# Performance work log

Measured on AMD Instinct MI355X. Metric: run time of the kernel, lower is better.

Reference implementation:

```python
import jax, jax.numpy as jnp
import numpy as np

B, S, H, D, M = 4, 512, 768, 24, 96
OUT_HID = 2 * max(128, H // 2)  # 768

def setup_inputs() -> dict:
    key = jax.random.key(0)
    ks = jax.random.split(key, 10)
    g = lambda k, shp, s=0.02: (jax.random.normal(k, shp, jnp.float32) * s)
    return {
        'H_j': jax.random.normal(ks[0], (B, S, H), jnp.float32),
        'H_i': jax.random.normal(ks[1], (B, S, H), jnp.float32),
        'attn_mask': jnp.ones((B, S), jnp.float32),
        'p_j_w': g(ks[2], (D, H)),
        'p_i_w': g(ks[3], (D, H)),
        's_w1': g(ks[4], (M, 4 * D)),
        's_b1': jnp.zeros((M,), jnp.float32),
        's_w2': g(ks[5], (1, M)),
        's_b2': jnp.zeros((1,), jnp.float32),
        'v_w1': g(ks[6], (OUT_HID, 3 * H)),
        'v_b1': jnp.zeros((OUT_HID,), jnp.float32),
        'v_w2': g(ks[7], (H, OUT_HID)),
        'v_b2': jnp.zeros((H,), jnp.float32),
        'alpha': jnp.asarray(0.05, jnp.float32),
    }

def reference(H_j, H_i, attn_mask, p_j_w, p_i_w, s_w1, s_b1, s_w2, s_b2,
              v_w1, v_b1, v_w2, v_b2, alpha):
    # Projections: [B,S,D]
    Zj = H_j @ p_j_w.T
    Zi = H_i @ p_i_w.T
    # score_mlp layer1 on concat([Zj_pair, Zi_pair, hadam, |diff|]) ==
    # sum of the 4 block-matmuls (block-split of W1 over the concat axis).
    Wa, Wb, Wc, Wd = jnp.split(s_w1, 4, axis=1)        # each [M, D]
    Zj_p = Zj[:, :, None, :]                            # [B,S,1,D]
    Zi_p = Zi[:, None, :, :]                            # [B,1,S,D]
    hid = (jnp.einsum('bsd,md->bsm', Zj, Wa)[:, :, None, :]
           + jnp.einsum('btd,md->btm', Zi, Wb)[:, None, :, :]
           + jnp.einsum('bstd,md->bstm', Zj_p * Zi_p, Wc)
           + jnp.einsum('bstd,md->bstm', jnp.abs(Zj_p - Zi_p), Wd)
           + s_b1)                                      # [B,S,S,M]
    logits = jnp.einsum('bstm,om->bst', jax.nn.relu(hid), s_w2)[..., :] + s_b2[0]  # [B,S,S]
    neg = jnp.finfo(logits.dtype).min
    logits = logits + (1.0 - attn_mask)[:, None, :] * neg  # mask over keys
    probs = jax.nn.softmax(logits, axis=-1)
    ctx = jnp.einsum('bst,bth->bsh', probs, H_i)           # [B,S,H]
    msg_in = jnp.concatenate([ctx, H_j, ctx * H_j], axis=-1)  # concat_hadam: [B,S,3H]
    msg = jax.nn.relu(msg_in @ v_w1.T + v_b1) @ v_w2.T + v_b2
    return alpha * msg  # dropout is identity in eval mode
```

## Files before the change

kernel.cpp:

```cpp
#include <hip/hip_runtime.h>
#include <hip/hip_bf16.h>
#include <math.h>

#define BB 4
#define SS 512
#define HH 768
#define DD 24
#define MM 96
#define OH 768
#define K3H 2304

typedef unsigned short u16;
typedef unsigned int u32;
typedef short bf16x8 __attribute__((ext_vector_type(8)));
typedef float f32x4 __attribute__((ext_vector_type(4)));
typedef u16 u16x4 __attribute__((ext_vector_type(4)));

#define OFF_A     0
#define F32_END   (OFF_A + BB*SS*MM)
#define MB_MSGIN  0
#define MB_H1     (MB_MSGIN + BB*SS*K3H)
#define MB_W1     (MB_H1    + BB*SS*OH)
#define MB_W2     (MB_W1    + OH*K3H)
#define MB_PROBS  (MB_W2    + OH*HH)
#define MB_HIT    (MB_PROBS + BB*SS*SS)
#define MB_ZJP    (MB_HIT   + BB*HH*SS)
#define MB_ZIP    (MB_ZJP   + BB*SS*32)
#define MB_WM     (MB_ZIP   + BB*SS*32)

__device__ inline u16 f2bf(float x) {
    union { float f; u32 u; } v; v.f = x;
    u32 r = v.u + 0x7fffu + ((v.u >> 16) & 1u);
    return (u16)(r >> 16);
}
__device__ inline u32 pk2bf(float lo, float hi) {
    return ((__float_as_uint(lo) + 0x8000u) >> 16) |
           ((__float_as_uint(hi) + 0x8000u) & 0xffff0000u);
}
__device__ inline void unpack8(bf16x8 v, float* f) {
    const u32* d = (const u32*)&v;
    #pragma unroll
    for (int i = 0; i < 4; ++i) {
        f[2*i]   = __uint_as_float(d[i] << 16);
        f[2*i+1] = __uint_as_float(d[i] & 0xffff0000u);
    }
}
__device__ inline void gl_lds16(const u16* g, u16* l) {
    __builtin_amdgcn_global_load_lds(
        (const __attribute__((address_space(1))) void*)g,
        (__attribute__((address_space(3))) void*)l, 16, 0, 0);
}

__global__ __launch_bounds__(256) void k_zproj(
    const float* __restrict__ Hj, const float* __restrict__ Hi,
    const float* __restrict__ pjw, const float* __restrict__ piw,
    const float* __restrict__ sw1, const float* __restrict__ sb1,
    u16* __restrict__ Zjp, u16* __restrict__ Zip, float* __restrict__ A)
{
    int bs = blockIdx.x;
    __shared__ float hj[HH], hi[HH], zj[DD], zi[DD];
    int tid = threadIdx.x;
    for (int i = tid; i < HH; i += 256) {
        hj[i] = Hj[(size_t)bs*HH + i];
        hi[i] = Hi[(size_t)bs*HH + i];
    }
    __syncthreads();
    int wid = tid >> 6, lane = tid & 63;
    for (int o = wid; o < 2*DD; o += 4) {
        int isJ = (o < DD); int d = isJ ? o : o - DD;
        const float* w = (isJ ? pjw : piw) + (size_t)d * HH;
        const float* x = isJ ? hj : hi;
        float acc = 0.f;
        #pragma unroll
        for (int k = 0; k < HH/64; ++k) { int h = lane + 64*k; acc = fmaf(x[h], w[h], acc); }
        #pragma unroll
        for (int off = 32; off > 0; off >>= 1) acc += __shfl_down(acc, off);
        if (lane == 0) { if (isJ) zj[d] = acc; else zi[d] = acc; }
    }
    __syncthreads();
    if (tid < 32)      Zjp[(size_t)bs*32 + tid] = (tid < DD) ? f2bf(zj[tid]) : (u16)0;
    else if (tid < 64) { int c = tid - 32; Zip[(size_t)bs*32 + c] = (c < DD) ? f2bf(zi[c]) : (u16)0; }
    if (tid < MM) {
        float acc = sb1[tid];
        #pragma unroll
        for (int d = 0; d < DD; ++d) acc = fmaf(zj[d], sw1[tid*96 + d], acc);
        A[(size_t)bs*MM + tid] = acc;
    }
}

__global__ __launch_bounds__(256) void k_wprep(
    const float* __restrict__ sw1, const float* __restrict__ vw1,
    const float* __restrict__ vw2,
    u16* __restrict__ Wm, u16* __restrict__ w1b, u16* __restrict__ w2b)
{
    int bx = blockIdx.x;
    if (bx == 0) {
        for (int i = threadIdx.x; i < MM*96; i += 256) {
            int m = i / 96, k = i % 96;
            float v = 0.f;
            if (k < 24)                 v = sw1[m*96 + 48 + k];
            else if (k >= 32 && k < 56) v = sw1[m*96 + 72 + (k - 32)];
            else if (k >= 64 && k < 88) v = sw1[m*96 + 24 + (k - 64)];
            Wm[i] = f2bf(v);
        }
        return;
    }
    int idx = bx - 1;
    const float* src; u16* dst;
    if (idx < 864) { src = vw1; dst = w1b; }
    else           { idx -= 864; src = vw2; dst = w2b; }
    int i = (idx*256 + threadIdx.x) * 8;
    float4 a = *(const float4*)&src[i];
    float4 c = *(const float4*)&src[i+4];
    u16x4 lo = { f2bf(a.x), f2bf(a.y), f2bf(a.z), f2bf(a.w) };
    u16x4 hi = { f2bf(c.x), f2bf(c.y), f2bf(c.z), f2bf(c.w) };
    *(u16x4*)&dst[i]   = lo;
    *(u16x4*)&dst[i+4] = hi;
}

__global__ __launch_bounds__(256) void k_pair_mfma(
    const u16* __restrict__ Zjp, const u16* __restrict__ Zip,
    const float* __restrict__ A, const u16* __restrict__ Wm,
    const float* __restrict__ sw2, const float* __restrict__ mask,
    u16* __restrict__ probsb)
{
    int blk = blockIdx.x; int b = blk >> 8; int s0 = (blk & 255) * 2;
    int tid = threadIdx.x, wave = tid >> 6, lane = tid & 63;
    int q = lane >> 4, l16 = lane & 15;
    int si = wave & 1, half = wave >> 1;
    int s = s0 + si, bs = b*SS + s;
    __shared__ __align__(16) u16 ZiS[SS*32];
    __shared__ float logits[2][SS];

    {
        const u16* zb = Zip + (size_t)b*SS*32;
        #pragma unroll
        for (int p = 0; p < 8; ++p) {
            int idx = p*256 + tid;
            int t = idx >> 2, c = idx & 3;
            int g = c ^ ((t + (t >> 2)) & 3);
            gl_lds16(zb + t*32 + g*8, ZiS + idx*8);
        }
    }

    bf16x8 zjf = *(const bf16x8*)&Zjp[(size_t)bs*32 + q*8];
    float zj[8]; unpack8(zjf, zj);
    bf16x8 afc[6], afd[6];
    #pragma unroll
    for (int mt = 0; mt < 6; ++mt) {
        const u16* wrow = &Wm[(mt*16 + l16)*96];
        bf16x8 wcf = *(const bf16x8*)&wrow[q*8];
        afd[mt]    = *(const bf16x8*)&wrow[32 + q*8];
        bf16x8 wbf = *(const bf16x8*)&wrow[64 + q*8];
        float fc[8], fb[8];
        unpack8(wcf, fc); unpack8(wbf, fb);
        u32 aval = (u32)f2bf(A[(size_t)bs*MM + mt*16 + l16]);
        union { u32 d[4]; bf16x8 v; } pk;
        #pragma unroll
        for (int i = 0; i < 4; ++i)
            pk.d[i] = pk2bf(fmaf(fc[2*i], zj[2*i], fb[2*i]),
                            fmaf(fc[2*i+1], zj[2*i+1], fb[2*i+1]));
        pk.d[0] = (q == 3) ? aval : pk.d[0];
        afc[mt] = pk.v;
    }
    float w2v[6][4];
    #pragma unroll
    for (int mt = 0; mt < 6; ++mt)
        #pragma unroll
        for (int r = 0; r < 4; ++r) w2v[mt][r] = sw2[mt*16 + q*4 + r];

    __syncthreads();

    for (int k = 0; k < 16; ++k) {
        int t0 = (half*16 + k) * 16;
        int trow = t0 + l16;
        int sw = q ^ ((trow + (trow >> 2)) & 3);
        bf16x8 zif = *(const bf16x8*)&ZiS[trow*32 + sw*8];
        float zi[8]; unpack8(zif, zi);
        union { u32 d[4]; bf16x8 v; } b1, b2;
        #pragma unroll
        for (int i = 0; i < 4; ++i)
            b1.d[i] = pk2bf(fabsf(zj[2*i] - zi[2*i]), fabsf(zj[2*i+1] - zi[2*i+1]));
        b2.v = zif;
        b2.d[0] = (q == 3) ? 0x3F80u : b2.d[0];
        f32x4 acc[6];
        #pragma unroll
        for (int mt = 0; mt < 6; ++mt) {
            f32x4 a = {};
            a = __builtin_amdgcn_mfma_f32_16x16x32_bf16(afc[mt], b2.v, a, 0,0,0);
            a = __builtin_amdgcn_mfma_f32_16x16x32_bf16(afd[mt], b1.v, a, 0,0,0);
            acc[mt] = a;
        }
        float p = 0.f;
        #pragma unroll
        for (int mt = 0; mt < 6; ++mt)
            #pragma unroll
            for (int r = 0; r < 4; ++r)
                p = fmaf(fmaxf(acc[mt][r], 0.f), w2v[mt][r], p);
        p += __shfl_xor(p, 16);
        p += __shfl_xor(p, 32);
        if (lane < 16) logits[si][t0 + lane] = p;
    }
    __syncthreads();

    if (wave < 2) {
        const float NEGF = -3.4028234663852886e38f;
        int bss = b*SS + s0 + wave;
        float l[8], e[8];
        float mx = -INFINITY;
        #pragma unroll
        for (int i = 0; i < 8; ++i) {
            int idx = lane + i*64;
            l[i] = logits[wave][idx] + (1.f - mask[b*SS + idx]) * NEGF;
            mx = fmaxf(mx, l[i]);
        }
        #pragma unroll
        for (int off = 32; off > 0; off >>= 1) mx = fmaxf(mx, __shfl_xor(mx, off));
        float sum = 0.f;
        #pragma unroll
        for (int i = 0; i < 8; ++i) { e[i] = __expf(l[i] - mx); sum += e[i]; }
        #pragma unroll
        for (int off = 32; off > 0; off >>= 1) sum += __shfl_xor(sum, off);
        float inv = 1.f / sum;
        #pragma unroll
        for (int i = 0; i < 8; ++i)
            probsb[(size_t)bss*SS + lane + i*64] = f2bf(e[i] * inv);
    }
}

__global__ __launch_bounds__(256) void k_hit(
    const float* __restrict__ Hi, u16* __restrict__ HiTb)
{
    int b = blockIdx.z; int t0 = blockIdx.x * 32; int h0 = blockIdx.y * 32;
    __shared__ float tile[32][33];
    int tx = threadIdx.x & 31, ty = threadIdx.x >> 5;
    for (int i = ty; i < 32; i += 8)
        tile[i][tx] = Hi[((size_t)(b*SS) + t0 + i)*HH + h0 + tx];
    __syncthreads();
    for (int i = ty; i < 32; i += 8)
        HiTb[((size_t)b*HH + h0 + i)*SS + t0 + tx] = f2bf(tile[tx][i]);
}

__global__ __launch_bounds__(256) void k_ctx_mfma(
    const u16* __restrict__ probsb, const u16* __restrict__ HiTb,
    const float* __restrict__ Hj, u16* __restrict__ msginb)
{
    int b = blockIdx.z;
    int h0 = blockIdx.x * 64;
    int s0 = blockIdx.y * 64;
    int tid = threadIdx.x;
    __shared__ __align__(16) u16 As[64*32];
    __shared__ __align__(16) u16 Bs[64*32];
    int row = tid >> 2, cs = tid & 3;
    int gchunk = cs ^ ((row >> 1) & 3);
    int wave = tid >> 6, lane = tid & 63;
    int wr = (wave >> 1) * 32, wc = (wave & 1) * 32;
    int q = lane >> 4, l16 = lane & 15;
    int sA = (l16 >> 1) & 3;
    f32x4 acc00 = {}, acc01 = {}, acc10 = {}, acc11 = {};
    const u16* ag = probsb + ((size_t)(b*SS) + s0 + row)*SS + gchunk*8;
    const u16* bg = HiTb + ((size_t)b*HH + h0 + row)*SS + gchunk*8;
    u16* lA = As + tid*8;
    u16* lB = Bs + tid*8;
    for (int k0 = 0; k0 < SS; k0 += 32) {
        gl_lds16(ag + k0, lA);
        gl_lds16(bg + k0, lB);
        __syncthreads();
        bf16x8 a0 = *(const bf16x8*)&As[(wr      + l16)*32 + (q^sA)*8];
        bf16x8 a1 = *(const bf16x8*)&As[(wr + 16 + l16)*32 + (q^sA)*8];
        bf16x8 b0 = *(const bf16x8*)&Bs[(wc      + l16)*32 + (q^sA)*8];
        bf16x8 b1 = *(const bf16x8*)&Bs[(wc + 16 + l16)*32 + (q^sA)*8];
        acc00 = __builtin_amdgcn_mfma_f32_16x16x32_bf16(a0, b0, acc00, 0,0,0);
        acc01 = __builtin_amdgcn_mfma_f32_16x16x32_bf16(a0, b1, acc01, 0,0,0);
        acc10 = __builtin_amdgcn_mfma_f32_16x16x32_bf16(a1, b0, acc10, 0,0,0);
        acc11 = __builtin_amdgcn_mfma_f32_16x16x32_bf16(a1, b1, acc11, 0,0,0);
        __syncthreads();
    }
    #pragma unroll
    for (int rt = 0; rt < 2; ++rt) {
        #pragma unroll
        for (int ct = 0; ct < 2; ++ct) {
            const f32x4* ac = rt ? (ct ? &acc11 : &acc10) : (ct ? &acc01 : &acc00);
            int h = h0 + wc + ct*16 + l16;
            #pragma unroll
            for (int r = 0; r < 4; ++r) {
                int s = s0 + wr + rt*16 + q*4 + r;
                float v = (*ac)[r];
                float hj = Hj[((size_t)(b*SS) + s)*HH + h];
                u16* mb = msginb + (size_t)(b*SS + s)*K3H + h;
                mb[0]    = f2bf(v);
                mb[HH]   = f2bf(hj);
                mb[2*HH] = f2bf(v * hj);
            }
        }
    }
}

__global__ __launch_bounds__(256) void k_mfma_gemm1(
    const u16* __restrict__ Abf, const u16* __restrict__ Bbf,
    const float* __restrict__ bias, u16* __restrict__ Cbf)
{
    int o0 = blockIdx.x * 64;
    int n0 = blockIdx.y * 64;
    int tid = threadIdx.x;
    __shared__ __align__(16) u16 As[64*32];
    __shared__ __align__(16) u16 Bs[64*32];
    int row = tid >> 2, cs = tid & 3;
    int gchunk = cs ^ ((row >> 1) & 3);
    int wave = tid >> 6, lane = tid & 63;
    int wr = (wave >> 1) * 32, wc = (wave & 1) * 32;
    int q = lane >> 4, l16 = lane & 15;
    int sA = (l16 >> 1) & 3;
    f32x4 acc00 = {}, acc01 = {}, acc10 = {}, acc11 = {};
    const u16* ag = Abf + (size_t)(n0 + row)*K3H + gchunk*8;
    const u16* bg = Bbf + (size_t)(o0 + row)*K3H + gchunk*8;
    u16* lA = As + tid*8;
    u16* lB = Bs + tid*8;
    for (int k0 = 0; k0 < K3H; k0 += 32) {
        gl_lds16(ag + k0, lA);
        gl_lds16(bg + k0, lB);
        __syncthreads();
        bf16x8 a0 = *(const bf16x8*)&As[(wr      + l16)*32 + (q^sA)*8];
        bf16x8 a1 = *(const bf16x8*)&As[(wr + 16 + l16)*32 + (q^sA)*8];
        bf16x8 b0 = *(const bf16x8*)&Bs[(wc      + l16)*32 + (q^sA)*8];
        bf16x8 b1 = *(const bf16x8*)&Bs[(wc + 16 + l16)*32 + (q^sA)*8];
        acc00 = __builtin_amdgcn_mfma_f32_16x16x32_bf16(a0, b0, acc00, 0,0,0);
        acc01 = __builtin_amdgcn_mfma_f32_16x16x32_bf16(a0, b1, acc01, 0,0,0);
        acc10 = __builtin_amdgcn_mfma_f32_16x16x32_bf16(a1, b0, acc10, 0,0,0);
        acc11 = __builtin_amdgcn_mfma_f32_16x16x32_bf16(a1, b1, acc11, 0,0,0);
        __syncthreads();
    }
    #pragma unroll
    for (int rt = 0; rt < 2; ++rt) {
        #pragma unroll
        for (int ct = 0; ct < 2; ++ct) {
            const f32x4* ac = rt ? (ct ? &acc11 : &acc10) : (ct ? &acc01 : &acc00);
            int o = o0 + wc + ct*16 + l16;
            float bv = bias[o];
            #pragma unroll
            for (int r = 0; r < 4; ++r) {
                int m = n0 + wr + rt*16 + q*4 + r;
                Cbf[(size_t)m*OH + o] = f2bf(fmaxf((*ac)[r] + bv, 0.f));
            }
        }
    }
}

__global__ __launch_bounds__(256) void k_mfma_gemm2(
    const u16* __restrict__ Abf, const u16* __restrict__ Bbf,
    const float* __restrict__ bias, const float* __restrict__ alpha,
    float* __restrict__ out)
{
    int o0 = blockIdx.x * 64;
    int n0 = blockIdx.y * 64;
    int tid = threadIdx.x;
    __shared__ __align__(16) u16 As[64*32];
    __shared__ __align__(16) u16 Bs[64*32];
    int row = tid >> 2, cs = tid & 3;
    int gchunk = cs ^ ((row >> 1) & 3);
    int wave = tid >> 6, lane = tid & 63;
    int wr = (wave >> 1) * 32, wc = (wave & 1) * 32;
    int q = lane >> 4, l16 = lane & 15;
    int sA = (l16 >> 1) & 3;
    f32x4 acc00 = {}, acc01 = {}, acc10 = {}, acc11 = {};
    const u16* ag = Abf + (size_t)(n0 + row)*OH + gchunk*8;
    const u16* bg = Bbf + (size_t)(o0 + row)*OH + gchunk*8;
    u16* lA = As + tid*8;
    u16* lB = Bs + tid*8;
    for (int k0 = 0; k0 < OH; k0 += 32) {
        gl_lds16(ag + k0, lA);
        gl_lds16(bg + k0, lB);
        __syncthreads();
        bf16x8 a0 = *(const bf16x8*)&As[(wr      + l16)*32 + (q^sA)*8];
        bf16x8 a1 = *(const bf16x8*)&As[(wr + 16 + l16)*32 + (q^sA)*8];
        bf16x8 b0 = *(const bf16x8*)&Bs[(wc      + l16)*32 + (q^sA)*8];
        bf16x8 b1 = *(const bf16x8*)&Bs[(wc + 16 + l16)*32 + (q^sA)*8];
        acc00 = __builtin_amdgcn_mfma_f32_16x16x32_bf16(a0, b0, acc00, 0,0,0);
        acc01 = __builtin_amdgcn_mfma_f32_16x16x32_bf16(a0, b1, acc01, 0,0,0);
        acc10 = __builtin_amdgcn_mfma_f32_16x16x32_bf16(a1, b0, acc10, 0,0,0);
        acc11 = __builtin_amdgcn_mfma_f32_16x16x32_bf16(a1, b1, acc11, 0,0,0);
        __syncthreads();
    }
    float al = alpha[0];
    #pragma unroll
    for (int rt = 0; rt < 2; ++rt) {
        #pragma unroll
        for (int ct = 0; ct < 2; ++ct) {
            const f32x4* ac = rt ? (ct ? &acc11 : &acc10) : (ct ? &acc01 : &acc00);
            int o = o0 + wc + ct*16 + l16;
            float bv = bias[o];
            #pragma unroll
            for (int r = 0; r < 4; ++r) {
                int m = n0 + wr + rt*16 + q*4 + r;
                out[(size_t)m*HH + o] = al * ((*ac)[r] + bv);
            }
        }
    }
}

extern "C" void kernel_launch(void* const* d_in, const int* in_sizes, int n_in,
                              void* d_out, int out_size, void* d_ws, size_t ws_size,
                              hipStream_t stream) {
    const float* Hj    = (const float*)d_in[0];
    const float* Hi    = (const float*)d_in[1];
    const float* amask = (const float*)d_in[2];
    const float* pjw   = (const float*)d_in[3];
    const float* piw   = (const float*)d_in[4];
    const float* sw1   = (const float*)d_in[5];
    const float* sb1   = (const float*)d_in[6];
    const float* sw2   = (const float*)d_in[7];
    const float* sb2   = (const float*)d_in[8];
    const float* vw1   = (const float*)d_in[9];
    const float* vb1   = (const float*)d_in[10];
    const float* vw2   = (const float*)d_in[11];
    const float* vb2   = (const float*)d_in[12];
    const float* alpha = (const float*)d_in[13];
    float* out = (float*)d_out;
    (void)sb2;

    float* ws   = (float*)d_ws;
    float* A    = ws + OFF_A;
    u16* bfbase = (u16*)(ws + F32_END);
    u16* msginb = bfbase + MB_MSGIN;
    u16* h1b    = bfbase + MB_H1;
    u16* w1b    = bfbase + MB_W1;
    u16* w2b    = bfbase + MB_W2;
    u16* probsb = bfbase + MB_PROBS;
    u16* hitb   = bfbase + MB_HIT;
    u16* zjp    = bfbase + MB_ZJP;
    u16* zip    = bfbase + MB_ZIP;
    u16* wm     = bfbase + MB_WM;

    k_zproj<<<BB*SS, 256, 0, stream>>>(Hj, Hi, pjw, piw, sw1, sb1, zjp, zip, A);
    k_wprep<<<1 + 864 + 288, 256, 0, stream>>>(sw1, vw1, vw2, wm, w1b, w2b);
    k_hit<<<dim3(SS/32, HH/32, BB), 256, 0, stream>>>(Hi, hitb);
    k_pair_mfma<<<BB*SS/2, 256, 0, stream>>>(zjp, zip, A, wm, sw2, amask, probsb);
    k_ctx_mfma<<<dim3(HH/64, SS/64, BB), 256, 0, stream>>>(probsb, hitb, Hj, msginb);
    k_mfma_gemm1<<<dim3(OH/64, BB*SS/64), 256, 0, stream>>>(msginb, w1b, vb1, h1b);
    k_mfma_gemm2<<<dim3(HH/64, BB*SS/64), 256, 0, stream>>>(h1b, w2b, vb2, alpha, out);
}
```

Baseline: 204.1 us.

## Replace projection kernel with MFMA GEMM, widen GEMM K-tiles, vectorize transpose

The per-row scalar projection kernel is replaced by an MFMA-based GEMM that computes Zj/Zi in bf16 and also derives the A term through a small MFMA against a prepacked bf16 Wa block, stored as bf16. The ctx and both MLP GEMMs move from 32-wide to 64-wide K tiles with an 8-chunk XOR swizzle, which halves the number of barrier round trips. The Hi transpose now uses 64x64 tiles with a bf16 LDS tile and 16-byte stores. The risks are extra bf16 rounding on the projections and A, low occupancy in the projection GEMM (64 blocks), and larger LDS use per GEMM block.

```diff
diff --git a/kernel.cpp b/kernel.cpp
--- a/kernel.cpp
+++ b/kernel.cpp
@@ -16,8 +16,6 @@
 typedef float f32x4 __attribute__((ext_vector_type(4)));
 typedef u16 u16x4 __attribute__((ext_vector_type(4)));
 
-#define OFF_A     0
-#define F32_END   (OFF_A + BB*SS*MM)
 #define MB_MSGIN  0
 #define MB_H1     (MB_MSGIN + BB*SS*K3H)
 #define MB_W1     (MB_H1    + BB*SS*OH)
@@ -27,6 +25,8 @@
 #define MB_ZJP    (MB_HIT   + BB*HH*SS)
 #define MB_ZIP    (MB_ZJP   + BB*SS*32)
 #define MB_WM     (MB_ZIP   + BB*SS*32)
+#define MB_WAB    (MB_WM    + MM*96)
+#define MB_AB     (MB_WAB   + MM*32)
 
 __device__ inline u16 f2bf(float x) {
     union { float f; u32 u; } v; v.f = x;
@@ -50,48 +50,15 @@
         (const __attribute__((address_space(1))) void*)g,
         (__attribute__((address_space(3))) void*)l, 16, 0, 0);
 }
-
-__global__ __launch_bounds__(256) void k_zproj(
-    const float* __restrict__ Hj, const float* __restrict__ Hi,
-    const float* __restrict__ pjw, const float* __restrict__ piw,
-    const float* __restrict__ sw1, const float* __restrict__ sb1,
-    u16* __restrict__ Zjp, u16* __restrict__ Zip, float* __restrict__ A)
-{
-    int bs = blockIdx.x;
-    __shared__ float hj[HH], hi[HH], zj[DD], zi[DD];
-    int tid = threadIdx.x;
-    for (int i = tid; i < HH; i += 256) {
-        hj[i] = Hj[(size_t)bs*HH + i];
-        hi[i] = Hi[(size_t)bs*HH + i];
-    }
-    __syncthreads();
-    int wid = tid >> 6, lane = tid & 63;
-    for (int o = wid; o < 2*DD; o += 4) {
-        int isJ = (o < DD); int d = isJ ? o : o - DD;
-        const float* w = (isJ ? pjw : piw) + (size_t)d * HH;
-        const float* x = isJ ? hj : hi;
-        float acc = 0.f;
-        #pragma unroll
-        for (int k = 0; k < HH/64; ++k) { int h = lane + 64*k; acc = fmaf(x[h], w[h], acc); }
-        #pragma unroll
-        for (int off = 32; off > 0; off >>= 1) acc += __shfl_down(acc, off);
-        if (lane == 0) { if (isJ) zj[d] = acc; else zi[d] = acc; }
-    }
-    __syncthreads();
-    if (tid < 32)      Zjp[(size_t)bs*32 + tid] = (tid < DD) ? f2bf(zj[tid]) : (u16)0;
-    else if (tid < 64) { int c = tid - 32; Zip[(size_t)bs*32 + c] = (c < DD) ? f2bf(zi[c]) : (u16)0; }
-    if (tid < MM) {
-        float acc = sb1[tid];
-        #pragma unroll
-        for (int d = 0; d < DD; ++d) acc = fmaf(zj[d], sw1[tid*96 + d], acc);
-        A[(size_t)bs*MM + tid] = acc;
-    }
+__device__ inline bf16x8 frag64(const u16* X, int r, int g) {
+    return *(const bf16x8*)&X[(r*8 + (g ^ (r & 7)))*8];
 }
 
 __global__ __launch_bounds__(256) void k_wprep(
     const float* __restrict__ sw1, const float* __restrict__ vw1,
     const float* __restrict__ vw2,
-    u16* __restrict__ Wm, u16* __restrict__ w1b, u16* __restrict__ w2b)
+    u16* __restrict__ Wm, u16* __restrict__ Wab,
+    u16* __restrict__ w1b, u16* __restrict__ w2b)
 {
     int bx = blockIdx.x;
     if (bx == 0) {
@@ -102,6 +69,10 @@
             else if (k >= 32 && k < 56) v = sw1[m*96 + 72 + (k - 32)];
             else if (k >= 64 && k < 88) v = sw1[m*96 + 24 + (k - 64)];
             Wm[i] = f2bf(v);
+        }
+        for (int i = threadIdx.x; i < MM*32; i += 256) {
+            int m = i >> 5, k = i & 31;
+            Wab[i] = (k < 24) ? f2bf(sw1[m*96 + k]) : (u16)0;
         }
         return;
     }
@@ -118,9 +89,92 @@
     *(u16x4*)&dst[i+4] = hi;
 }
 
+__global__ __launch_bounds__(256) void k_zgemm(
+    const float* __restrict__ Hj, const float* __restrict__ Hi,
+    const float* __restrict__ pjw, const float* __restrict__ piw,
+    const float* __restrict__ sw1, const float* __restrict__ sb1,
+    const u16* __restrict__ Wab,
+    u16* __restrict__ Zjp, u16* __restrict__ Zip, u16* __restrict__ Ab)
+{
+    int isJ = (blockIdx.y == 0);
+    const float* H = isJ ? Hj : Hi;
+    const float* P = isJ ? pjw : piw;
+    u16* Zout = isJ ? Zjp : Zip;
+    int n0 = blockIdx.x * 64;
+    int tid = threadIdx.x, wave = tid >> 6, lane = tid & 63;
+    int q = lane >> 4, l16 = lane & 15;
+    __shared__ __align__(16) u16 As[64*32];
+    __shared__ __align__(16) u16 Bs[32*32];
+    __shared__ __align__(16) u16 zb[64*32];
+
+    { int i = tid; Bs[(24 + (i >> 5))*32 + (i & 31)] = 0; }
+
+    int arow = tid >> 2, aseg = tid & 3;
+    const float* ah = H + (size_t)(n0 + arow)*HH + aseg*8;
+    int brow = tid >> 2, bseg = tid & 3;
+    const float* bh = P + (size_t)brow*HH + bseg*8;
+    int adst = arow*32 + ((aseg ^ (arow & 3))*8);
+    int bdst = brow*32 + ((bseg ^ (brow & 3))*8);
+
+    float4 xa = *(const float4*)(ah);
+    float4 ya = *(const float4*)(ah + 4);
+    float4 xb = {}, yb = {};
+    if (tid < 96) { xb = *(const float4*)(bh); yb = *(const float4*)(bh + 4); }
+
+    f32x4 acc0 = {}, acc1 = {};
+    int ga = q ^ (l16 & 3);
+    for (int k0 = 0; k0 < HH; k0 += 32) {
+        { u32* w = (u32*)&As[adst];
+          w[0] = pk2bf(xa.x, xa.y); w[1] = pk2bf(xa.z, xa.w);
+          w[2] = pk2bf(ya.x, ya.y); w[3] = pk2bf(ya.z, ya.w); }
+        if (tid < 96) {
+          u32* w = (u32*)&Bs[bdst];
+          w[0] = pk2bf(xb.x, xb.y); w[1] = pk2bf(xb.z, xb.w);
+          w[2] = pk2bf(yb.x, yb.y); w[3] = pk2bf(yb.z, yb.w); }
+        float4 nxa = {}, nya = {}, nxb = {}, nyb = {};
+        if (k0 + 32 < HH) {
+            nxa = *(const float4*)(ah + k0 + 32);
+            nya = *(const float4*)(ah + k0 + 36);
+            if (tid < 96) { nxb = *(const float4*)(bh + k0 + 32);
+                            nyb = *(const float4*)(bh + k0 + 36); }
+        }
+        __syncthreads();
+        bf16x8 af = *(const bf16x8*)&As[(wave*16 + l16)*32 + ga*8];
+        bf16x8 b0 = *(const bf16x8*)&Bs[l16*32 + ga*8];
+        bf16x8 b1 = *(const bf16x8*)&Bs[(16 + l16)*32 + ga*8];
+        acc0 = __builtin_amdgcn_mfma_f32_16x16x32_bf16(af, b0, acc0, 0,0,0);
+        acc1 = __builtin_amdgcn_mfma_f32_16x16x32_bf16(af, b1, acc1, 0,0,0);
+        __syncthreads();
+        xa = nxa; ya = nya; xb = nxb; yb = nyb;
+    }
+    #pragma unroll
+    for (int r = 0; r < 4; ++r) {
+        zb[(wave*16 + q*4 + r)*32 + l16]      = f2bf(acc0[r]);
+        zb[(wave*16 + q*4 + r)*32 + 16 + l16] = f2bf(acc1[r]);
+    }
+    __syncthreads();
+    { uint4 v = *(const uint4*)&zb[tid*8];
+      *(uint4*)&Zout[(size_t)n0*32 + tid*8] = v; }
+    if (isJ) {
+        bf16x8 af = *(const bf16x8*)&zb[(wave*16 + l16)*32 + q*8];
+        #pragma unroll
+        for (int nt = 0; nt < 6; ++nt) {
+            bf16x8 bw = *(const bf16x8*)&Wab[(nt*16 + l16)*32 + q*8];
+            f32x4 a = {};
+            a = __builtin_amdgcn_mfma_f32_16x16x32_bf16(af, bw, a, 0,0,0);
+            float bv = sb1[nt*16 + l16];
+            #pragma unroll
+            for (int r = 0; r < 4; ++r) {
+                int bs = n0 + wave*16 + q*4 + r;
+                Ab[(size_t)bs*MM + nt*16 + l16] = f2bf(a[r] + bv);
+            }
+        }
+    }
+}
+
 __global__ __launch_bounds__(256) void k_pair_mfma(
     const u16* __restrict__ Zjp, const u16* __restrict__ Zip,
-    const float* __restrict__ A, const u16* __restrict__ Wm,
+    const u16* __restrict__ Ab, const u16* __restrict__ Wm,
     const float* __restrict__ sw2, const float* __restrict__ mask,
     u16* __restrict__ probsb)
 {
@@ -154,7 +208,7 @@
         bf16x8 wbf = *(const bf16x8*)&wrow[64 + q*8];
         float fc[8], fb[8];
         unpack8(wcf, fc); unpack8(wbf, fb);
-        u32 aval = (u32)f2bf(A[(size_t)bs*MM + mt*16 + l16]);
+        u32 aval = (u32)Ab[(size_t)bs*MM + mt*16 + l16];
         union { u32 d[4]; bf16x8 v; } pk;
         #pragma unroll
         for (int i = 0; i < 4; ++i)
@@ -231,14 +285,25 @@
 __global__ __launch_bounds__(256) void k_hit(
     const float* __restrict__ Hi, u16* __restrict__ HiTb)
 {
-    int b = blockIdx.z; int t0 = blockIdx.x * 32; int h0 = blockIdx.y * 32;
-    __shared__ float tile[32][33];
-    int tx = threadIdx.x & 31, ty = threadIdx.x >> 5;
-    for (int i = ty; i < 32; i += 8)
-        tile[i][tx] = Hi[((size_t)(b*SS) + t0 + i)*HH + h0 + tx];
+    int b = blockIdx.z, t0 = blockIdx.x*64, h0 = blockIdx.y*64;
+    __shared__ u16 tile[64*74];
+    int r = threadIdx.x >> 2, cs = threadIdx.x & 3;
+    const float* src = Hi + ((size_t)(b*SS) + t0 + r)*HH + h0 + cs*16;
+    u16* dst = &tile[r*74 + cs*16];
+    #pragma unroll
+    for (int i = 0; i < 4; ++i) {
+        float4 v = *(const float4*)(src + i*4);
+        *(u32*)&dst[i*4]     = pk2bf(v.x, v.y);
+        *(u32*)&dst[i*4 + 2] = pk2bf(v.z, v.w);
+    }
     __syncthreads();
-    for (int i = ty; i < 32; i += 8)
-        HiTb[((size_t)b*HH + h0 + i)*SS + t0 + tx] = f2bf(tile[tx][i]);
+    int hr = threadIdx.x >> 2;
+    u16 outv[16];
+    #pragma unroll
+    for (int i = 0; i < 16; ++i) outv[i] = tile[(cs*16 + i)*74 + hr];
+    u16* o = HiTb + ((size_t)b*HH + h0 + hr)*SS + t0 + cs*16;
+    *(uint4*)o       = *(const uint4*)&outv[0];
+    *(uint4*)(o + 8) = *(const uint4*)&outv[8];
 }
 
 __global__ __launch_bounds__(256) void k_ctx_mfma(
@@ -249,43 +314,45 @@
     int h0 = blockIdx.x * 64;
     int s0 = blockIdx.y * 64;
     int tid = threadIdx.x;
-    __shared__ __align__(16) u16 As[64*32];
-    __shared__ __align__(16) u16 Bs[64*32];
-    int row = tid >> 2, cs = tid & 3;
-    int gchunk = cs ^ ((row >> 1) & 3);
+    __shared__ __align__(16) u16 As[64*64];
+    __shared__ __align__(16) u16 Bs[64*64];
     int wave = tid >> 6, lane = tid & 63;
     int wr = (wave >> 1) * 32, wc = (wave & 1) * 32;
     int q = lane >> 4, l16 = lane & 15;
-    int sA = (l16 >> 1) & 3;
-    f32x4 acc00 = {}, acc01 = {}, acc10 = {}, acc11 = {};
-    const u16* ag = probsb + ((size_t)(b*SS) + s0 + row)*SS + gchunk*8;
-    const u16* bg = HiTb + ((size_t)b*HH + h0 + row)*SS + gchunk*8;
-    u16* lA = As + tid*8;
-    u16* lB = Bs + tid*8;
-    for (int k0 = 0; k0 < SS; k0 += 32) {
-        gl_lds16(ag + k0, lA);
-        gl_lds16(bg + k0, lB);
-        __syncthreads();
-        bf16x8 a0 = *(const bf16x8*)&As[(wr      + l16)*32 + (q^sA)*8];
-        bf16x8 a1 = *(const bf16x8*)&As[(wr + 16 + l16)*32 + (q^sA)*8];
-        bf16x8 b0 = *(const bf16x8*)&Bs[(wc      + l16)*32 + (q^sA)*8];
-        bf16x8 b1 = *(const bf16x8*)&Bs[(wc + 16 + l16)*32 + (q^sA)*8];
-        acc00 = __builtin_amdgcn_mfma_f32_16x16x32_bf16(a0, b0, acc00, 0,0,0);
-        acc01 = __builtin_amdgcn_mfma_f32_16x16x32_bf16(a0, b1, acc01, 0,0,0);
-        acc10 = __builtin_amdgcn_mfma_f32_16x16x32_bf16(a1, b0, acc10, 0,0,0);
-        acc11 = __builtin_amdgcn_mfma_f32_16x16x32_bf16(a1, b1, acc11, 0,0,0);
+    f32x4 acc[2][2] = {};
+    const u16* ag = probsb + ((size_t)(b*SS) + s0)*SS;
+    const u16* bg = HiTb + ((size_t)b*HH + h0)*SS;
+    for (int k0 = 0; k0 < SS; k0 += 64) {
+        #pragma unroll
+        for (int p = 0; p < 2; ++p) {
+            int sl = p*256 + tid; int rr = sl >> 3, gi = sl & 7, g = gi ^ (rr & 7);
+            gl_lds16(ag + (size_t)rr*SS + k0 + g*8, As + sl*8);
+            gl_lds16(bg + (size_t)rr*SS + k0 + g*8, Bs + sl*8);
+        }
+        __syncthreads();
+        #pragma unroll
+        for (int ks = 0; ks < 2; ++ks) {
+            int g = ks*4 + q;
+            bf16x8 a0 = frag64(As, wr + l16, g);
+            bf16x8 a1 = frag64(As, wr + 16 + l16, g);
+            bf16x8 b0 = frag64(Bs, wc + l16, g);
+            bf16x8 b1 = frag64(Bs, wc + 16 + l16, g);
+            acc[0][0] = __builtin_amdgcn_mfma_f32_16x16x32_bf16(a0, b0, acc[0][0], 0,0,0);
+            acc[0][1] = __builtin_amdgcn_mfma_f32_16x16x32_bf16(a0, b1, acc[0][1], 0,0,0);
+            acc[1][0] = __builtin_amdgcn_mfma_f32_16x16x32_bf16(a1, b0, acc[1][0], 0,0,0);
+            acc[1][1] = __builtin_amdgcn_mfma_f32_16x16x32_bf16(a1, b1, acc[1][1], 0,0,0);
+        }
         __syncthreads();
     }
     #pragma unroll
     for (int rt = 0; rt < 2; ++rt) {
         #pragma unroll
         for (int ct = 0; ct < 2; ++ct) {
-            const f32x4* ac = rt ? (ct ? &acc11 : &acc10) : (ct ? &acc01 : &acc00);
             int h = h0 + wc + ct*16 + l16;
             #pragma unroll
             for (int r = 0; r < 4; ++r) {
                 int s = s0 + wr + rt*16 + q*4 + r;
-                float v = (*ac)[r];
+                float v = acc[rt][ct][r];
                 float hj = Hj[((size_t)(b*SS) + s)*HH + h];
                 u16* mb = msginb + (size_t)(b*SS + s)*K3H + h;
                 mb[0]    = f2bf(v);
@@ -303,44 +370,46 @@
     int o0 = blockIdx.x * 64;
     int n0 = blockIdx.y * 64;
     int tid = threadIdx.x;
-    __shared__ __align__(16) u16 As[64*32];
-    __shared__ __align__(16) u16 Bs[64*32];
-    int row = tid >> 2, cs = tid & 3;
-    int gchunk = cs ^ ((row >> 1) & 3);
+    __shared__ __align__(16) u16 As[64*64];
+    __shared__ __align__(16) u16 Bs[64*64];
     int wave = tid >> 6, lane = tid & 63;
     int wr = (wave >> 1) * 32, wc = (wave & 1) * 32;
     int q = lane >> 4, l16 = lane & 15;
-    int sA = (l16 >> 1) & 3;
-    f32x4 acc00 = {}, acc01 = {}, acc10 = {}, acc11 = {};
-    const u16* ag = Abf + (size_t)(n0 + row)*K3H + gchunk*8;
-    const u16* bg = Bbf + (size_t)(o0 + row)*K3H + gchunk*8;
-    u16* lA = As + tid*8;
-    u16* lB = Bs + tid*8;
-    for (int k0 = 0; k0 < K3H; k0 += 32) {
-        gl_lds16(ag + k0, lA);
-        gl_lds16(bg + k0, lB);
-        __syncthreads();
-        bf16x8 a0 = *(const bf16x8*)&As[(wr      + l16)*32 + (q^sA)*8];
-        bf16x8 a1 = *(const bf16x8*)&As[(wr + 16 + l16)*32 + (q^sA)*8];
-        bf16x8 b0 = *(const bf16x8*)&Bs[(wc      + l16)*32 + (q^sA)*8];
-        bf16x8 b1 = *(const bf16x8*)&Bs[(wc + 16 + l16)*32 + (q^sA)*8];
-        acc00 = __builtin_amdgcn_mfma_f32_16x16x32_bf16(a0, b0, acc00, 0,0,0);
-        acc01 = __builtin_amdgcn_mfma_f32_16x16x32_bf16(a0, b1, acc01, 0,0,0);
-        acc10 = __builtin_amdgcn_mfma_f32_16x16x32_bf16(a1, b0, acc10, 0,0,0);
-        acc11 = __builtin_amdgcn_mfma_f32_16x16x32_bf16(a1, b1, acc11, 0,0,0);
+    f32x4 acc[2][2] = {};
+    const u16* ag = Abf + (size_t)n0*K3H;
+    const u16* bg = Bbf + (size_t)o0*K3H;
+    for (int k0 = 0; k0 < K3H; k0 += 64) {
+        #pragma unroll
+        for (int p = 0; p < 2; ++p) {
+            int sl = p*256 + tid; int rr = sl >> 3, gi = sl & 7, g = gi ^ (rr & 7);
+            gl_lds16(ag + (size_t)rr*K3H + k0 + g*8, As + sl*8);
+            gl_lds16(bg + (size_t)rr*K3H + k0 + g*8, Bs + sl*8);
+        }
+        __syncthreads();
+        #pragma unroll
+        for (int ks = 0; ks < 2; ++ks) {
+            int g = ks*4 + q;
+            bf16x8 a0 = frag64(As, wr + l16, g);
+            bf16x8 a1 = frag64(As, wr + 16 + l16, g);
+            bf16x8 b0 = frag64(Bs, wc + l16, g);
+            bf16x8 b1 = frag64(Bs, wc + 16 + l16, g);
+            acc[0][0] = __builtin_amdgcn_mfma_f32_16x16x32_bf16(a0, b0, acc[0][0], 0,0,0);
+            acc[0][1] = __builtin_amdgcn_mfma_f32_16x16x32_bf16(a0, b1, acc[0][1], 0,0,0);
+            acc[1][0] = __builtin_amdgcn_mfma_f32_16x16x32_bf16(a1, b0, acc[1][0], 0,0,0);
+            acc[1][1] = __builtin_amdgcn_mfma_f32_16x16x32_bf16(a1, b1, acc[1][1], 0,0,0);
+        }
         __syncthreads();
     }
     #pragma unroll
     for (int rt = 0; rt < 2; ++rt) {
         #pragma unroll
         for (int ct = 0; ct < 2; ++ct) {
-            const f32x4* ac = rt ? (ct ? &acc11 : &acc10) : (ct ? &acc01 : &acc00);
             int o = o0 + wc + ct*16 + l16;
             float bv = bias[o];
             #pragma unroll
             for (int r = 0; r < 4; ++r) {
                 int m = n0 + wr + rt*16 + q*4 + r;
-                Cbf[(size_t)m*OH + o] = f2bf(fmaxf((*ac)[r] + bv, 0.f));
+                Cbf[(size_t)m*OH + o] = f2bf(fmaxf(acc[rt][ct][r] + bv, 0.f));
             }
         }
     }
@@ -354,31 +423,34 @@
     int o0 = blockIdx.x * 64;
     int n0 = blockIdx.y * 64;
     int tid = threadIdx.x;
-    __shared__ __align__(16) u16 As[64*32];
-    __shared__ __align__(16) u16 Bs[64*32];
-    int row = tid >> 2, cs = tid & 3;
-    int gchunk = cs ^ ((row >> 1) & 3);
+    __shared__ __align__(16) u16 As[64*64];
+    __shared__ __align__(16) u16 Bs[64*64];
     int wave = tid >> 6, lane = tid & 63;
     int wr = (wave >> 1) * 32, wc = (wave & 1) * 32;
     int q = lane >> 4, l16 = lane & 15;
-    int sA = (l16 >> 1) & 3;
-    f32x4 acc00 = {}, acc01 = {}, acc10 = {}, acc11 = {};
-    const u16* ag = Abf + (size_t)(n0 + row)*OH + gchunk*8;
-    const u16* bg = Bbf + (size_t)(o0 + row)*OH + gchunk*8;
-    u16* lA = As + tid*8;
-    u16* lB = Bs + tid*8;
-    for (int k0 = 0; k0 < OH; k0 += 32) {
-        gl_lds16(ag + k0, lA);
-        gl_lds16(bg + k0, lB);
-        __syncthreads();
-        bf16x8 a0 = *(const bf16x8*)&As[(wr      + l16)*32 + (q^sA)*8];
-        bf16x8 a1 = *(const bf16x8*)&As[(wr + 16 + l16)*32 + (q^sA)*8];
-        bf16x8 b0 = *(const bf16x8*)&Bs[(wc      + l16)*32 + (q^sA)*8];
-        bf16x8 b1 = *(const bf16x8*)&Bs[(wc + 16 + l16)*32 + (q^sA)*8];
-        acc00 = __builtin_amdgcn_mfma_f32_16x16x32_bf16(a0, b0, acc00, 0,0,0);
-        acc01 = __builtin_amdgcn_mfma_f32_16x16x32_bf16(a0, b1, acc01, 0,0,0);
-        acc10 = __builtin_amdgcn_mfma_f32_16x16x32_bf16(a1, b0, acc10, 0,0,0);
-        acc11 = __builtin_amdgcn_mfma_f32_16x16x32_bf16(a1, b1, acc11, 0,0,0);
+    f32x4 acc[2][2] = {};
+    const u16* ag = Abf + (size_t)n0*OH;
+    const u16* bg = Bbf + (size_t)o0*OH;
+    for (int k0 = 0; k0 < OH; k0 += 64) {
+        #pragma unroll
+        for (int p = 0; p < 2; ++p) {
+            int sl = p*256 + tid; int rr = sl >> 3, gi = sl & 7, g = gi ^ (rr & 7);
+            gl_lds16(ag + (size_t)rr*OH + k0 + g*8, As + sl*8);
+            gl_lds16(bg + (size_t)rr*OH + k0 + g*8, Bs + sl*8);
+        }
+        __syncthreads();
+        #pragma unroll
+        for (int ks = 0; ks < 2; ++ks) {
+            int g = ks*4 + q;
+            bf16x8 a0 = frag64(As, wr + l16, g);
+            bf16x8 a1 = frag64(As, wr + 16 + l16, g);
+            bf16x8 b0 = frag64(Bs, wc + l16, g);
+            bf16x8 b1 = frag64(Bs, wc + 16 + l16, g);
+            acc[0][0] = __builtin_amdgcn_mfma_f32_16x16x32_bf16(a0, b0, acc[0][0], 0,0,0);
+            acc[0][1] = __builtin_amdgcn_mfma_f32_16x16x32_bf16(a0, b1, acc[0][1], 0,0,0);
+            acc[1][0] = __builtin_amdgcn_mfma_f32_16x16x32_bf16(a1, b0, acc[1][0], 0,0,0);
+            acc[1][1] = __builtin_amdgcn_mfma_f32_16x16x32_bf16(a1, b1, acc[1][1], 0,0,0);
+        }
         __syncthreads();
     }
     float al = alpha[0];
@@ -386,13 +458,12 @@
     for (int rt = 0; rt < 2; ++rt) {
         #pragma unroll
         for (int ct = 0; ct < 2; ++ct) {
-            const f32x4* ac = rt ? (ct ? &acc11 : &acc10) : (ct ? &acc01 : &acc00);
             int o = o0 + wc + ct*16 + l16;
             float bv = bias[o];
             #pragma unroll
             for (int r = 0; r < 4; ++r) {
                 int m = n0 + wr + rt*16 + q*4 + r;
-                out[(size_t)m*HH + o] = al * ((*ac)[r] + bv);
+                out[(size_t)m*HH + o] = al * (acc[rt][ct][r] + bv);
             }
         }
     }
@@ -418,9 +489,7 @@
     float* out = (float*)d_out;
     (void)sb2;
 
-    float* ws   = (float*)d_ws;
-    float* A    = ws + OFF_A;
-    u16* bfbase = (u16*)(ws + F32_END);
+    u16* bfbase = (u16*)d_ws;
     u16* msginb = bfbase + MB_MSGIN;
     u16* h1b    = bfbase + MB_H1;
     u16* w1b    = bfbase + MB_W1;
@@ -430,11 +499,13 @@
     u16* zjp    = bfbase + MB_ZJP;
     u16* zip    = bfbase + MB_ZIP;
     u16* wm     = bfbase + MB_WM;
-
-    k_zproj<<<BB*SS, 256, 0, stream>>>(Hj, Hi, pjw, piw, sw1, sb1, zjp, zip, A);
-    k_wprep<<<1 + 864 + 288, 256, 0, stream>>>(sw1, vw1, vw2, wm, w1b, w2b);
-    k_hit<<<dim3(SS/32, HH/32, BB), 256, 0, stream>>>(Hi, hitb);
-    k_pair_mfma<<<BB*SS/2, 256, 0, stream>>>(zjp, zip, A, wm, sw2, amask, probsb);
+    u16* wab    = bfbase + MB_WAB;
+    u16* ab     = bfbase + MB_AB;
+
+    k_wprep<<<1 + 864 + 288, 256, 0, stream>>>(sw1, vw1, vw2, wm, wab, w1b, w2b);
+    k_zgemm<<<dim3(32, 2), 256, 0, stream>>>(Hj, Hi, pjw, piw, sw1, sb1, wab, zjp, zip, ab);
+    k_hit<<<dim3(SS/64, HH/64, BB), 256, 0, stream>>>(Hi, hitb);
+    k_pair_mfma<<<BB*SS/2, 256, 0, stream>>>(zjp, zip, ab, wm, sw2, amask, probsb);
     k_ctx_mfma<<<dim3(HH/64, SS/64, BB), 256, 0, stream>>>(probsb, hitb, Hj, msginb);
     k_mfma_gemm1<<<dim3(OH/64, BB*SS/64), 256, 0, stream>>>(msginb, w1b, vb1, h1b);
     k_mfma_gemm2<<<dim3(HH/64, BB*SS/64), 256, 0, stream>>>(h1b, w2b, vb2, alpha, out);
```

New measurement: 194.5 us. 4.7% less time.
